# Kernel optimization log

Hardware: AMD Instinct MI355X
Metric: run time of the kernel (lower is better)

Reference implementation:

```python
import jax, jax.numpy as jnp
import numpy as np

B, N, D, K, DSPACE, NFREQ = 4, 4096, 256, 16, 3, 5
BN_EPS = 1e-5


def setup_inputs() -> dict:
    key = jax.random.key(0)
    ks = jax.random.split(key, 12)
    s = 1.0 / np.sqrt(D)
    pe_in = DSPACE * 2 * NFREQ + DSPACE  # 33
    return {
        "xyz": jax.random.normal(ks[0], (B, N, DSPACE), jnp.float32),
        "feats": jax.random.normal(ks[1], (B, N, D), jnp.float32),
        "w_q": jax.random.uniform(ks[2], (D, D), jnp.float32, -s, s),
        "w_k": jax.random.uniform(ks[3], (D, D), jnp.float32, -s, s),
        "w_v": jax.random.uniform(ks[4], (D, D), jnp.float32, -s, s),
        "g_w1": jax.random.uniform(ks[5], (D, D), jnp.float32, -s, s),
        "g_b1": jax.random.uniform(ks[6], (D,), jnp.float32, -s, s),
        "g_w2": jax.random.uniform(ks[7], (D, D), jnp.float32, -s, s),
        "g_b2": jax.random.uniform(ks[8], (D,), jnp.float32, -s, s),
        "pe_w": jax.random.uniform(ks[9], (D, pe_in), jnp.float32, -s, s),
        "pe_b": jax.random.uniform(ks[10], (D,), jnp.float32, -s, s),
        "bn_w": jnp.ones((D,), jnp.float32),
        "bn_b": jnp.zeros((D,), jnp.float32),
    }


def _gather_knn(points, idx):
    # points [b,n,c], idx [b,n,k] -> [b,n,k,c]
    return jax.vmap(lambda p, i: p[i])(points, idx)


def reference(xyz, feats, w_q, w_k, w_v, g_w1, g_b1, g_w2, g_b2, pe_w, pe_b, bn_w, bn_b):
    # KNN (no grad in original): full pairwise sq-distance + top-k smallest
    dists = jnp.sum((xyz[:, :, None] - xyz[:, None]) ** 2, axis=-1)  # [b,n,n]
    _, knn_idx = jax.lax.top_k(-dists, K)  # [b,n,k], ascending distance
    knn_idx = jax.lax.stop_gradient(knn_idx)
    knn_xyz = jax.lax.stop_gradient(_gather_knn(xyz, knn_idx))  # [b,n,k,3]

    q = feats @ w_q.T                               # [b,n,d]
    k_g = _gather_knn(feats @ w_k.T, knn_idx)       # [b,n,k,d]
    v_g = _gather_knn(feats @ w_v.T, knn_idx)       # [b,n,k,d]

    pos_diff = xyz[:, :, None] - knn_xyz            # [b,n,k,3]
    freqs = jnp.linspace(1.0, 2.0 ** NFREQ, NFREQ).astype(pos_diff.dtype)
    embeds = [pos_diff]
    for f in freqs:
        embeds.append(jnp.sin(pos_diff * f))
        embeds.append(jnp.cos(pos_diff * f))
    pos_embed = jnp.concatenate(embeds, axis=-1)    # [b,n,k,33]
    pos_encode = pos_embed @ pe_w.T + pe_b          # [b,n,k,d]

    edges = q[:, :, None] - k_g + pos_encode        # [b,n,k,d]
    h = jax.nn.relu(edges @ g_w1.T + g_b1)
    attn = h @ g_w2.T + g_b2                        # [b,n,k,d]
    attn = jax.nn.softmax(attn, axis=-2)            # softmax over neighbors

    res = jnp.einsum('bnkf,bnkf->bnf', attn, v_g + pos_encode) + feats

    # BatchNorm1d over channel dim, training-mode batch stats (biased var)
    mean = jnp.mean(res, axis=(0, 1))
    var = jnp.var(res, axis=(0, 1))
    res = (res - mean) * jax.lax.rsqrt(var + BN_EPS) * bn_w + bn_b
    return res
```

## Files before the change

kernel.cpp:

```cpp
#include <hip/hip_runtime.h>

#define BB 4
#define NN 4096
#define DD 256
#define KK 16
#define PTS 2
#define SA 264

typedef __bf16 bf16;
typedef __attribute__((ext_vector_type(8))) __bf16 bf16x8;
typedef __attribute__((ext_vector_type(4))) __bf16 bf16x4;
typedef __attribute__((ext_vector_type(4))) float f32x4;

#define KNNB 4096
#define PROJB 256
#define PREPB 256

__global__ __launch_bounds__(256, 2) void setup_kernel(
    const float* __restrict__ xyz, const float* __restrict__ feats,
    const float* __restrict__ w_q, const float* __restrict__ w_k,
    const float* __restrict__ w_v, const float* __restrict__ g_w1,
    const float* __restrict__ g_w2, const float* __restrict__ pe_w,
    int* __restrict__ knn, bf16* __restrict__ qb, bf16* __restrict__ kfb,
    bf16* __restrict__ vfb, bf16* __restrict__ w1b, bf16* __restrict__ w2b,
    bf16* __restrict__ pwb, float* __restrict__ sums) {
  const int bid = blockIdx.x;
  const int t = threadIdx.x;
  __shared__ __align__(16) float smem[NN * 3];

  if (bid < KNNB) {
    const int row0 = bid * 4;
    const int b = row0 >> 12;
    const float* xb = xyz + (size_t)b * NN * 3;
    for (int e = t; e < NN * 3; e += 256) smem[e] = xb[e];
    __syncthreads();
    const int lane = t & 63;
    const int row = row0 + (t >> 6);
    const int i = row & (NN - 1);
    const float xi = smem[i * 3 + 0], yi = smem[i * 3 + 1], zi = smem[i * 3 + 2];
    unsigned long long cand[64];
#pragma unroll
    for (int c = 0; c < 64; ++c) {
      const int j = c * 64 + lane;
      const float dx = xi - smem[j * 3 + 0];
      const float dy = yi - smem[j * 3 + 1];
      const float dz = zi - smem[j * 3 + 2];
      const float d = dx * dx + dy * dy + dz * dz;
      const unsigned long long fb =
          (unsigned long long)(__float_as_uint(d)) + 1ull;
      cand[c] = (fb << 32) | (unsigned int)j;
    }
    unsigned long long gm[8];
#pragma unroll
    for (int g = 0; g < 8; ++g) {
      unsigned long long mn = cand[g * 8];
#pragma unroll
      for (int s = 1; s < 8; ++s)
        if (cand[g * 8 + s] < mn) mn = cand[g * 8 + s];
      gm[g] = mn;
    }
    unsigned int myj = 0u;
    for (int r = 0; r < KK; ++r) {
      unsigned long long lmin = gm[0];
#pragma unroll
      for (int g = 1; g < 8; ++g)
        if (gm[g] < lmin) lmin = gm[g];
#pragma unroll
      for (int off = 1; off < 64; off <<= 1) {
        const unsigned long long o = __shfl_xor(lmin, off);
        if (o < lmin) lmin = o;
      }
      if (lane == r) myj = (unsigned int)lmin;
#pragma unroll
      for (int g = 0; g < 8; ++g) {
        if (__ballot(gm[g] == lmin)) {
          unsigned long long nm = ~0ull;
#pragma unroll
          for (int s = 0; s < 8; ++s) {
            const unsigned long long v = cand[g * 8 + s];
            if (v > lmin && v < nm) nm = v;
          }
          if (gm[g] == lmin) gm[g] = nm;
        }
      }
    }
    if (lane < KK) knn[row * KK + lane] = (int)myj;
    return;
  }
  if (bid < KNNB + PROJB) {
    bf16(*fs)[SA] = (bf16(*)[SA])smem;
    const int lane = t & 63, wv = t >> 6;
    const int m = lane & 15, qd = lane >> 4;
    const size_t r0 = (size_t)(bid - KNNB) * 64;
    const float4* f4 = (const float4*)(feats + r0 * DD);
#pragma unroll
    for (int i = 0; i < 16; ++i) {
      const int e = i * 256 + t;
      const float4 v = f4[e];
      bf16x4 w;
      w[0] = (bf16)v.x; w[1] = (bf16)v.y; w[2] = (bf16)v.z; w[3] = (bf16)v.w;
      *(bf16x4*)&fs[e >> 6][(e & 63) * 4] = w;
    }
    __syncthreads();
    bf16x8 afrag[8];
#pragma unroll
    for (int f = 0; f < 8; ++f)
      afrag[f] = *(const bf16x8*)&fs[wv * 16 + m][f * 32 + qd * 8];
    const float* wmat[3] = {w_q, w_k, w_v};
    bf16* omat[3] = {qb, kfb, vfb};
    for (int mat = 0; mat < 3; ++mat) {
      const float* wb = wmat[mat];
      for (int nt = 0; nt < 16; ++nt) {
        const int n = nt * 16 + m;
        bf16x8 bfr[8];
#pragma unroll
        for (int f = 0; f < 8; ++f) {
          const float4 wa =
              *(const float4*)(wb + (size_t)n * DD + f * 32 + qd * 8);
          const float4 wc =
              *(const float4*)(wb + (size_t)n * DD + f * 32 + qd * 8 + 4);
          bf16x8 x;
          x[0] = (bf16)wa.x; x[1] = (bf16)wa.y; x[2] = (bf16)wa.z; x[3] = (bf16)wa.w;
          x[4] = (bf16)wc.x; x[5] = (bf16)wc.y; x[6] = (bf16)wc.z; x[7] = (bf16)wc.w;
          bfr[f] = x;
        }
        f32x4 c = {0.f, 0.f, 0.f, 0.f};
#pragma unroll
        for (int f = 0; f < 8; ++f)
          c = __builtin_amdgcn_mfma_f32_16x16x32_bf16(afrag[f], bfr[f], c, 0, 0, 0);
#pragma unroll
        for (int rr = 0; rr < 4; ++rr)
          omat[mat][(r0 + wv * 16 + qd * 4 + rr) * DD + n] = (bf16)c[rr];
      }
    }
    return;
  }
  {
    const int idx = (bid - (KNNB + PROJB)) * 256 + t;
    w1b[idx] = (bf16)g_w1[idx];
    w2b[idx] = (bf16)g_w2[idx];
    if (idx < 256 * 64) {
      const int n = idx >> 6, c = idx & 63;
      pwb[idx] = (c < 33) ? (bf16)pe_w[n * 33 + c] : (bf16)0.f;
    }
    if (idx < 2 * DD) sums[idx] = 0.f;
  }
}

__device__ __forceinline__ float embval(int c, float pd0, float pd1, float pd2) {
  if (c > 32) return 0.f;
  const int cm = c - 3;
  const int ax = (c < 3) ? c : cm % 3;
  const float pdv = (ax == 0) ? pd0 : ((ax == 1) ? pd1 : pd2);
  if (c < 3) return pdv;
  const int f = cm / 6;
  const float x = pdv * fmaf(7.75f, (float)f, 1.0f);
  return ((cm % 6) < 3) ? __sinf(x) : __cosf(x);
}

__global__ __launch_bounds__(256, 3) void edge_v9(
    const float* __restrict__ xyz, const float* __restrict__ feats,
    const bf16* __restrict__ qb, const bf16* __restrict__ kfb,
    const bf16* __restrict__ vfb, const int* __restrict__ knn,
    const bf16* __restrict__ w1b, const float* __restrict__ g_b1,
    const bf16* __restrict__ w2b, const float* __restrict__ g_b2,
    const bf16* __restrict__ pwb, const float* __restrict__ pe_b,
    float* __restrict__ res, float* __restrict__ sums,
    float* __restrict__ sumsq) {
  const int t = threadIdx.x;
  const int lane = t & 63;
  const int wv = t >> 6;
  const int m = lane & 15;
  const int qd = lane >> 4;
  const int row0 = blockIdx.x * PTS;
  const int b = row0 >> 12;

  __shared__ __align__(16) bf16 bufA[PTS][16][SA];
  __shared__ __align__(16) char un_s[PTS * 16 * SA * 2];
  bf16(*bufB)[16][SA] = (bf16(*)[16][SA])un_s;
  bf16(*kf_s)[16][SA] = (bf16(*)[16][SA])un_s;
  __shared__ __align__(16) bf16 vf_s[PTS][16][SA];
  __shared__ int js_s[PTS][16];

  if (t < PTS * 16) js_s[t >> 4][t & 15] = knn[(row0 + (t >> 4)) * KK + (t & 15)];
  __syncthreads();

#pragma unroll
  for (int i = 0; i < 4; ++i) {
    const int e = i * 256 + t;
    const int p = e >> 9, rem = e & 511;
    const int k = rem >> 5, ch = rem & 31;
    const size_t base = ((size_t)(b * NN + js_s[p][k])) * DD + ch * 8;
    *(bf16x8*)&kf_s[p][k][ch * 8] = *(const bf16x8*)(kfb + base);
    *(bf16x8*)&vf_s[p][k][ch * 8] = *(const bf16x8*)(vfb + base);
  }

  const float* xb = xyz + (size_t)b * NN * 3;
  bf16x8 ea0[PTS], ea1[PTS];
#pragma unroll
  for (int p = 0; p < PTS; ++p) {
    const int i = (row0 + p) & (NN - 1);
    const int j = js_s[p][m];
    const float pd0 = xb[i * 3 + 0] - xb[j * 3 + 0];
    const float pd1 = xb[i * 3 + 1] - xb[j * 3 + 1];
    const float pd2 = xb[i * 3 + 2] - xb[j * 3 + 2];
#pragma unroll
    for (int jj = 0; jj < 8; ++jj) {
      ea0[p][jj] = (bf16)embval(qd * 8 + jj, pd0, pd1, pd2);
      ea1[p][jj] = (bf16)embval(32 + qd * 8 + jj, pd0, pd1, pd2);
    }
  }
  __syncthreads();

  float pe_r[4][PTS][4];
#pragma unroll
  for (int tt = 0; tt < 4; ++tt) {
    const int n = wv * 64 + tt * 16 + m;
    const bf16x8 b0 = *(const bf16x8*)(pwb + (size_t)n * 64 + qd * 8);
    const bf16x8 b1 = *(const bf16x8*)(pwb + (size_t)n * 64 + 32 + qd * 8);
    const float bias = pe_b[n];
#pragma unroll
    for (int p = 0; p < PTS; ++p) {
      f32x4 c = {bias, bias, bias, bias};
      c = __builtin_amdgcn_mfma_f32_16x16x32_bf16(ea0[p], b0, c, 0, 0, 0);
      c = __builtin_amdgcn_mfma_f32_16x16x32_bf16(ea1[p], b1, c, 0, 0, 0);
      const float qv = (float)qb[(size_t)(row0 + p) * DD + n];
#pragma unroll
      for (int rr = 0; rr < 4; ++rr) {
        const int krow = qd * 4 + rr;
        bufA[p][krow][n] = (bf16)(qv - (float)kf_s[p][krow][n] + c[rr]);
        pe_r[tt][p][rr] = c[rr];
      }
    }
  }
  __syncthreads();

  {
    bf16x8 afrag[PTS][8];
#pragma unroll
    for (int p = 0; p < PTS; ++p)
#pragma unroll
      for (int f = 0; f < 8; ++f)
        afrag[p][f] = *(const bf16x8*)&bufA[p][m][f * 32 + qd * 8];
    for (int tt = 0; tt < 4; ++tt) {
      const int n = wv * 64 + tt * 16 + m;
      bf16x8 bfr[8];
#pragma unroll
      for (int f = 0; f < 8; ++f)
        bfr[f] = *(const bf16x8*)(w1b + (size_t)n * DD + f * 32 + qd * 8);
      const float bias = g_b1[n];
#pragma unroll
      for (int p = 0; p < PTS; ++p) {
        f32x4 c = {bias, bias, bias, bias};
#pragma unroll
        for (int f = 0; f < 8; ++f)
          c = __builtin_amdgcn_mfma_f32_16x16x32_bf16(afrag[p][f], bfr[f], c, 0, 0, 0);
#pragma unroll
        for (int rr = 0; rr < 4; ++rr)
          bufB[p][qd * 4 + rr][n] = (bf16)fmaxf(c[rr], 0.f);
      }
    }
  }
  __syncthreads();

  {
    bf16x8 afrag[PTS][8];
#pragma unroll
    for (int p = 0; p < PTS; ++p)
#pragma unroll
      for (int f = 0; f < 8; ++f)
        afrag[p][f] = *(const bf16x8*)&bufB[p][m][f * 32 + qd * 8];
#pragma unroll
    for (int tt = 0; tt < 4; ++tt) {
      const int n = wv * 64 + tt * 16 + m;
      bf16x8 bfr[8];
#pragma unroll
      for (int f = 0; f < 8; ++f)
        bfr[f] = *(const bf16x8*)(w2b + (size_t)n * DD + f * 32 + qd * 8);
      const float bias = g_b2[n];
      float bs = 0.f, bs2 = 0.f;
#pragma unroll
      for (int p = 0; p < PTS; ++p) {
        f32x4 c = {bias, bias, bias, bias};
#pragma unroll
        for (int f = 0; f < 8; ++f)
          c = __builtin_amdgcn_mfma_f32_16x16x32_bf16(afrag[p][f], bfr[f], c, 0, 0, 0);
        float mx = fmaxf(fmaxf(c[0], c[1]), fmaxf(c[2], c[3]));
        mx = fmaxf(mx, __shfl_xor(mx, 16));
        mx = fmaxf(mx, __shfl_xor(mx, 32));
        float e[4], den = 0.f;
#pragma unroll
        for (int rr = 0; rr < 4; ++rr) {
          e[rr] = __expf(c[rr] - mx);
          den += e[rr];
        }
        den += __shfl_xor(den, 16);
        den += __shfl_xor(den, 32);
        float num = 0.f;
#pragma unroll
        for (int rr = 0; rr < 4; ++rr) {
          const float vpe =
              (float)vf_s[p][qd * 4 + rr][n] + pe_r[tt][p][rr];
          num += e[rr] * vpe;
        }
        num += __shfl_xor(num, 16);
        num += __shfl_xor(num, 32);
        if (qd == 0) {
          const size_t o = (size_t)(row0 + p) * DD + n;
          const float out = num / den + feats[o];
          res[o] = out;
          bs += out;
          bs2 += out * out;
        }
      }
      if (qd == 0) {
        atomicAdd(&sums[n], bs);
        atomicAdd(&sumsq[n], bs2);
      }
    }
  }
}

__global__ __launch_bounds__(256) void bn_apply(float* __restrict__ out,
                                                const float* __restrict__ sums,
                                                const float* __restrict__ sumsq,
                                                const float* __restrict__ bn_w,
                                                const float* __restrict__ bn_b) {
  const int idx = blockIdx.x * 256 + threadIdx.x;
  const int c = idx & (DD - 1);
  const float inv_n = 1.f / (float)(BB * NN);
  const float mean = sums[c] * inv_n;
  const float var = sumsq[c] * inv_n - mean * mean;
  const float v = out[idx];
  out[idx] = (v - mean) * rsqrtf(var + 1e-5f) * bn_w[c] + bn_b[c];
}

extern "C" void kernel_launch(void* const* d_in, const int* in_sizes, int n_in,
                              void* d_out, int out_size, void* d_ws,
                              size_t ws_size, hipStream_t stream) {
  (void)in_sizes; (void)n_in; (void)out_size; (void)ws_size;
  const float* xyz = (const float*)d_in[0];
  const float* feats = (const float*)d_in[1];
  const float* w_q = (const float*)d_in[2];
  const float* w_k = (const float*)d_in[3];
  const float* w_v = (const float*)d_in[4];
  const float* g_w1 = (const float*)d_in[5];
  const float* g_b1 = (const float*)d_in[6];
  const float* g_w2 = (const float*)d_in[7];
  const float* g_b2 = (const float*)d_in[8];
  const float* pe_w = (const float*)d_in[9];
  const float* pe_b = (const float*)d_in[10];
  const float* bn_w = (const float*)d_in[11];
  const float* bn_b = (const float*)d_in[12];
  float* out = (float*)d_out;

  const int BN = BB * NN;
  char* w = (char*)d_ws;
  int* knn = (int*)w;       w += (size_t)BN * KK * 4;
  bf16* qb = (bf16*)w;      w += (size_t)BN * DD * 2;
  bf16* kfb = (bf16*)w;     w += (size_t)BN * DD * 2;
  bf16* vfb = (bf16*)w;     w += (size_t)BN * DD * 2;
  float* sums = (float*)w;  w += DD * 4;
  float* sumsq = (float*)w; w += DD * 4;
  bf16* w1b = (bf16*)w;     w += (size_t)DD * DD * 2;
  bf16* w2b = (bf16*)w;     w += (size_t)DD * DD * 2;
  bf16* pwb = (bf16*)w;     w += (size_t)DD * 64 * 2;

  setup_kernel<<<KNNB + PROJB + PREPB, 256, 0, stream>>>(
      xyz, feats, w_q, w_k, w_v, g_w1, g_w2, pe_w, knn, qb, kfb, vfb, w1b, w2b,
      pwb, sums);
  edge_v9<<<BN / PTS, 256, 0, stream>>>(xyz, feats, qb, kfb, vfb, knn, w1b,
                                        g_b1, w2b, g_b2, pwb, pe_b, out, sums,
                                        sumsq);
  bn_apply<<<BN, 256, 0, stream>>>(out, sums, sumsq, bn_w, bn_b);
}
```

Baseline: 619.1 us.

## Split setup into KNN, projection and prep kernels with register-light KNN

The fused setup kernel is split into three separate kernels so that each gets its own launch bounds and shared-memory footprint. The KNN kernel stores xyz in structure-of-arrays shared memory and handles 8 rows per block. It keeps only 8 group minima per lane, not 64 candidates, and recomputes distances for a group when that group's minimum is consumed. This is meant to cut register pressure and raise occupancy (launch bounds 3) at the cost of extra distance arithmetic and two more kernel launches.

```diff
diff --git a/kernel.cpp b/kernel.cpp
--- a/kernel.cpp
+++ b/kernel.cpp
@@ -12,53 +12,57 @@
 typedef __attribute__((ext_vector_type(4))) __bf16 bf16x4;
 typedef __attribute__((ext_vector_type(4))) float f32x4;
 
-#define KNNB 4096
+#define KROWS 8
+#define KNNB (BB * NN / KROWS)
 #define PROJB 256
 #define PREPB 256
 
-__global__ __launch_bounds__(256, 2) void setup_kernel(
-    const float* __restrict__ xyz, const float* __restrict__ feats,
-    const float* __restrict__ w_q, const float* __restrict__ w_k,
-    const float* __restrict__ w_v, const float* __restrict__ g_w1,
-    const float* __restrict__ g_w2, const float* __restrict__ pe_w,
-    int* __restrict__ knn, bf16* __restrict__ qb, bf16* __restrict__ kfb,
-    bf16* __restrict__ vfb, bf16* __restrict__ w1b, bf16* __restrict__ w2b,
-    bf16* __restrict__ pwb, float* __restrict__ sums) {
-  const int bid = blockIdx.x;
+__device__ __forceinline__ unsigned long long distpack(float xi, float yi,
+                                                       float zi, float xj,
+                                                       float yj, float zj,
+                                                       int j) {
+  const float dx = xi - xj, dy = yi - yj, dz = zi - zj;
+  const float d = fmaf(dz, dz, fmaf(dy, dy, dx * dx));
+  return (((unsigned long long)__float_as_uint(d) + 1ull) << 32) |
+         (unsigned int)j;
+}
+
+__global__ __launch_bounds__(256, 3) void knn_kernel(
+    const float* __restrict__ xyz, int* __restrict__ knn) {
   const int t = threadIdx.x;
-  __shared__ __align__(16) float smem[NN * 3];
-
-  if (bid < KNNB) {
-    const int row0 = bid * 4;
-    const int b = row0 >> 12;
-    const float* xb = xyz + (size_t)b * NN * 3;
-    for (int e = t; e < NN * 3; e += 256) smem[e] = xb[e];
-    __syncthreads();
-    const int lane = t & 63;
-    const int row = row0 + (t >> 6);
+  const int lane = t & 63;
+  const int wv = t >> 6;
+  const int row_base = blockIdx.x * KROWS;
+  const int b = row_base >> 12;
+
+  __shared__ float xs[NN], ys[NN], zs[NN];
+  const float* xb = xyz + (size_t)b * NN * 3;
+  for (int e = t; e < NN * 3; e += 256) {
+    const int idx = e / 3;
+    const int ax = e - idx * 3;
+    const float v = xb[e];
+    if (ax == 0) xs[idx] = v;
+    else if (ax == 1) ys[idx] = v;
+    else zs[idx] = v;
+  }
+  __syncthreads();
+
+  for (int rr = 0; rr < KROWS / 4; ++rr) {
+    const int row = row_base + rr * 4 + wv;
     const int i = row & (NN - 1);
-    const float xi = smem[i * 3 + 0], yi = smem[i * 3 + 1], zi = smem[i * 3 + 2];
-    unsigned long long cand[64];
+    const float xi = xs[i], yi = ys[i], zi = zs[i];
+
+    unsigned long long gm[8];
+#pragma unroll
+    for (int g = 0; g < 8; ++g) gm[g] = ~0ull;
 #pragma unroll
     for (int c = 0; c < 64; ++c) {
       const int j = c * 64 + lane;
-      const float dx = xi - smem[j * 3 + 0];
-      const float dy = yi - smem[j * 3 + 1];
-      const float dz = zi - smem[j * 3 + 2];
-      const float d = dx * dx + dy * dy + dz * dz;
-      const unsigned long long fb =
-          (unsigned long long)(__float_as_uint(d)) + 1ull;
-      cand[c] = (fb << 32) | (unsigned int)j;
-    }
-    unsigned long long gm[8];
-#pragma unroll
-    for (int g = 0; g < 8; ++g) {
-      unsigned long long mn = cand[g * 8];
-#pragma unroll
-      for (int s = 1; s < 8; ++s)
-        if (cand[g * 8 + s] < mn) mn = cand[g * 8 + s];
-      gm[g] = mn;
-    }
+      const unsigned long long v =
+          distpack(xi, yi, zi, xs[j], ys[j], zs[j], j);
+      if (v < gm[c >> 3]) gm[c >> 3] = v;
+    }
+
     unsigned int myj = 0u;
     for (int r = 0; r < KK; ++r) {
       unsigned long long lmin = gm[0];
@@ -77,7 +81,9 @@
           unsigned long long nm = ~0ull;
 #pragma unroll
           for (int s = 0; s < 8; ++s) {
-            const unsigned long long v = cand[g * 8 + s];
+            const int j = (g * 8 + s) * 64 + lane;
+            const unsigned long long v =
+                distpack(xi, yi, zi, xs[j], ys[j], zs[j], j);
             if (v > lmin && v < nm) nm = v;
           }
           if (gm[g] == lmin) gm[g] = nm;
@@ -85,66 +91,74 @@
       }
     }
     if (lane < KK) knn[row * KK + lane] = (int)myj;
-    return;
-  }
-  if (bid < KNNB + PROJB) {
-    bf16(*fs)[SA] = (bf16(*)[SA])smem;
-    const int lane = t & 63, wv = t >> 6;
-    const int m = lane & 15, qd = lane >> 4;
-    const size_t r0 = (size_t)(bid - KNNB) * 64;
-    const float4* f4 = (const float4*)(feats + r0 * DD);
-#pragma unroll
-    for (int i = 0; i < 16; ++i) {
-      const int e = i * 256 + t;
-      const float4 v = f4[e];
-      bf16x4 w;
-      w[0] = (bf16)v.x; w[1] = (bf16)v.y; w[2] = (bf16)v.z; w[3] = (bf16)v.w;
-      *(bf16x4*)&fs[e >> 6][(e & 63) * 4] = w;
-    }
-    __syncthreads();
-    bf16x8 afrag[8];
-#pragma unroll
-    for (int f = 0; f < 8; ++f)
-      afrag[f] = *(const bf16x8*)&fs[wv * 16 + m][f * 32 + qd * 8];
-    const float* wmat[3] = {w_q, w_k, w_v};
-    bf16* omat[3] = {qb, kfb, vfb};
-    for (int mat = 0; mat < 3; ++mat) {
-      const float* wb = wmat[mat];
-      for (int nt = 0; nt < 16; ++nt) {
-        const int n = nt * 16 + m;
-        bf16x8 bfr[8];
-#pragma unroll
-        for (int f = 0; f < 8; ++f) {
-          const float4 wa =
-              *(const float4*)(wb + (size_t)n * DD + f * 32 + qd * 8);
-          const float4 wc =
-              *(const float4*)(wb + (size_t)n * DD + f * 32 + qd * 8 + 4);
-          bf16x8 x;
-          x[0] = (bf16)wa.x; x[1] = (bf16)wa.y; x[2] = (bf16)wa.z; x[3] = (bf16)wa.w;
-          x[4] = (bf16)wc.x; x[5] = (bf16)wc.y; x[6] = (bf16)wc.z; x[7] = (bf16)wc.w;
-          bfr[f] = x;
-        }
-        f32x4 c = {0.f, 0.f, 0.f, 0.f};
-#pragma unroll
-        for (int f = 0; f < 8; ++f)
-          c = __builtin_amdgcn_mfma_f32_16x16x32_bf16(afrag[f], bfr[f], c, 0, 0, 0);
-#pragma unroll
-        for (int rr = 0; rr < 4; ++rr)
-          omat[mat][(r0 + wv * 16 + qd * 4 + rr) * DD + n] = (bf16)c[rr];
-      }
-    }
-    return;
-  }
-  {
-    const int idx = (bid - (KNNB + PROJB)) * 256 + t;
-    w1b[idx] = (bf16)g_w1[idx];
-    w2b[idx] = (bf16)g_w2[idx];
-    if (idx < 256 * 64) {
-      const int n = idx >> 6, c = idx & 63;
-      pwb[idx] = (c < 33) ? (bf16)pe_w[n * 33 + c] : (bf16)0.f;
-    }
-    if (idx < 2 * DD) sums[idx] = 0.f;
-  }
+  }
+}
+
+__global__ __launch_bounds__(256, 2) void proj_kernel(
+    const float* __restrict__ feats, const float* __restrict__ w_q,
+    const float* __restrict__ w_k, const float* __restrict__ w_v,
+    bf16* __restrict__ qb, bf16* __restrict__ kfb, bf16* __restrict__ vfb) {
+  const int t = threadIdx.x;
+  __shared__ __align__(16) bf16 fs[64][SA];
+  const int lane = t & 63, wv = t >> 6;
+  const int m = lane & 15, qd = lane >> 4;
+  const size_t r0 = (size_t)blockIdx.x * 64;
+  const float4* f4 = (const float4*)(feats + r0 * DD);
+#pragma unroll
+  for (int i = 0; i < 16; ++i) {
+    const int e = i * 256 + t;
+    const float4 v = f4[e];
+    bf16x4 w;
+    w[0] = (bf16)v.x; w[1] = (bf16)v.y; w[2] = (bf16)v.z; w[3] = (bf16)v.w;
+    *(bf16x4*)&fs[e >> 6][(e & 63) * 4] = w;
+  }
+  __syncthreads();
+  bf16x8 afrag[8];
+#pragma unroll
+  for (int f = 0; f < 8; ++f)
+    afrag[f] = *(const bf16x8*)&fs[wv * 16 + m][f * 32 + qd * 8];
+  const float* wmat[3] = {w_q, w_k, w_v};
+  bf16* omat[3] = {qb, kfb, vfb};
+  for (int mat = 0; mat < 3; ++mat) {
+    const float* wb = wmat[mat];
+    for (int nt = 0; nt < 16; ++nt) {
+      const int n = nt * 16 + m;
+      bf16x8 bfr[8];
+#pragma unroll
+      for (int f = 0; f < 8; ++f) {
+        const float4 wa =
+            *(const float4*)(wb + (size_t)n * DD + f * 32 + qd * 8);
+        const float4 wc =
+            *(const float4*)(wb + (size_t)n * DD + f * 32 + qd * 8 + 4);
+        bf16x8 x;
+        x[0] = (bf16)wa.x; x[1] = (bf16)wa.y; x[2] = (bf16)wa.z; x[3] = (bf16)wa.w;
+        x[4] = (bf16)wc.x; x[5] = (bf16)wc.y; x[6] = (bf16)wc.z; x[7] = (bf16)wc.w;
+        bfr[f] = x;
+      }
+      f32x4 c = {0.f, 0.f, 0.f, 0.f};
+#pragma unroll
+      for (int f = 0; f < 8; ++f)
+        c = __builtin_amdgcn_mfma_f32_16x16x32_bf16(afrag[f], bfr[f], c, 0, 0, 0);
+#pragma unroll
+      for (int rr = 0; rr < 4; ++rr)
+        omat[mat][(r0 + wv * 16 + qd * 4 + rr) * DD + n] = (bf16)c[rr];
+    }
+  }
+}
+
+__global__ __launch_bounds__(256) void prep_kernel(
+    const float* __restrict__ g_w1, const float* __restrict__ g_w2,
+    const float* __restrict__ pe_w, bf16* __restrict__ w1b,
+    bf16* __restrict__ w2b, bf16* __restrict__ pwb,
+    float* __restrict__ sums) {
+  const int idx = blockIdx.x * 256 + threadIdx.x;
+  w1b[idx] = (bf16)g_w1[idx];
+  w2b[idx] = (bf16)g_w2[idx];
+  if (idx < 256 * 64) {
+    const int n = idx >> 6, c = idx & 63;
+    pwb[idx] = (c < 33) ? (bf16)pe_w[n * 33 + c] : (bf16)0.f;
+  }
+  if (idx < 2 * DD) sums[idx] = 0.f;
 }
 
 __device__ __forceinline__ float embval(int c, float pd0, float pd1, float pd2) {
@@ -186,7 +200,7 @@
   __syncthreads();
 
 #pragma unroll
-  for (int i = 0; i < 4; ++i) {
+  for (int i = 0; i < PTS * 2; ++i) {
     const int e = i * 256 + t;
     const int p = e >> 9, rem = e & 511;
     const int k = rem >> 5, ch = rem & 31;
@@ -366,9 +380,10 @@
   bf16* w2b = (bf16*)w;     w += (size_t)DD * DD * 2;
   bf16* pwb = (bf16*)w;     w += (size_t)DD * 64 * 2;
 
-  setup_kernel<<<KNNB + PROJB + PREPB, 256, 0, stream>>>(
-      xyz, feats, w_q, w_k, w_v, g_w1, g_w2, pe_w, knn, qb, kfb, vfb, w1b, w2b,
-      pwb, sums);
+  knn_kernel<<<KNNB, 256, 0, stream>>>(xyz, knn);
+  proj_kernel<<<PROJB, 256, 0, stream>>>(feats, w_q, w_k, w_v, qb, kfb, vfb);
+  prep_kernel<<<PREPB, 256, 0, stream>>>(g_w1, g_w2, pe_w, w1b, w2b, pwb,
+                                         sums);
   edge_v9<<<BN / PTS, 256, 0, stream>>>(xyz, feats, qb, kfb, vfb, knn, w1b,
                                         g_b1, w2b, g_b2, pwb, pe_b, out, sums,
                                         sumsq);
```

After: 982.2 us. 1.59x slower.
